# Kernel tuning notes

Measured on AMD Instinct MI355X. Metric: run time of the kernel, lower is better.

## Reference

```python
import jax, jax.numpy as jnp
import numpy as np

N_NODES = 50000
IN_DIM = 128
OUT_DIM = 128
HEADS = 4
HEAD_DIM = OUT_DIM // HEADS
N_EDGES = 800000
LN_EPS = 1e-5
NEG_SLOPE = 0.2


def setup_inputs() -> dict:
    key = jax.random.key(0)
    ks = jax.random.split(key, 8)
    x = jax.random.normal(ks[0], (N_NODES, IN_DIM), dtype=jnp.float32)
    edge_index = jax.random.randint(ks[1], (2, N_EDGES), 0, N_NODES, dtype=jnp.int64)
    s = 1.0 / np.sqrt(IN_DIM)
    W = jax.random.uniform(ks[2], (IN_DIM, HEADS * HEAD_DIM), jnp.float32, -s, s)
    att_src = jax.random.uniform(ks[3], (HEADS, HEAD_DIM), jnp.float32, -s, s)
    att_dst = jax.random.uniform(ks[4], (HEADS, HEAD_DIM), jnp.float32, -s, s)
    bias = jnp.zeros((OUT_DIM,), jnp.float32)
    gamma = jnp.ones((OUT_DIM,), jnp.float32)
    beta = jnp.zeros((OUT_DIM,), jnp.float32)
    return {"x": x, "edge_index": edge_index, "W": W, "att_src": att_src,
            "att_dst": att_dst, "bias": bias, "gamma": gamma, "beta": beta}


def reference(x, edge_index, W, att_src, att_dst, bias, gamma, beta):
    N = x.shape[0]
    H, C = att_src.shape
    # add self-loops (PyG GATConv default)
    loops = jnp.arange(N, dtype=edge_index.dtype)
    src = jnp.concatenate([edge_index[0], loops])  # [E+N]
    dst = jnp.concatenate([edge_index[1], loops])

    h = (x @ W).reshape(N, H, C)                      # [N,H,C]
    a_src = jnp.einsum('nhc,hc->nh', h, att_src)      # [N,H]
    a_dst = jnp.einsum('nhc,hc->nh', h, att_dst)

    e = jax.nn.leaky_relu(a_src[src] + a_dst[dst], NEG_SLOPE)   # [E+N,H]
    emax = jax.ops.segment_max(e, dst, num_segments=N)          # [N,H]
    ex = jnp.exp(e - emax[dst])
    denom = jax.ops.segment_sum(ex, dst, num_segments=N)
    alpha = ex / denom[dst]                                     # [E+N,H]

    msg = h[src] * alpha[:, :, None]                            # [E+N,H,C]
    out = jax.ops.segment_sum(msg, dst, num_segments=N).reshape(N, H * C) + bias

    # LayerNorm
    mu = out.mean(-1, keepdims=True)
    var = ((out - mu) ** 2).mean(-1, keepdims=True)
    hn = (out - mu) / jnp.sqrt(var + LN_EPS) * gamma + beta

    # residual is Identity (in_dim == out_dim); GELU exact; dropout = eval identity
    return jax.nn.gelu(hn + x, approximate=False)
```

## Files before the change

### kernel.cpp

```cpp
#include <hip/hip_runtime.h>
#include <math.h>

#define N_NODES 50000
#define HEADS 4
#define NEG_SLOPE 0.2f
#define LN_EPS 1e-5f
#define SLOTS 80
#define GR 64
#define EPB 2048
#define DSH 8
#define NB 196
#define CAP 40

typedef short short8 __attribute__((ext_vector_type(8)));
typedef float f32x4 __attribute__((ext_vector_type(4)));


__device__ __forceinline__ short f2bf(float f) {
    unsigned u = __float_as_uint(f);
    return (short)((u + 0x7fffu + ((u >> 16) & 1u)) >> 16);
}

__device__ __forceinline__ int detect_is64(const int* __restrict__ ei, int t, int* s_flag) {
    if (t < 64) {
        int nz = (ei[2 * t + 1] != 0) ? 1 : 0;
        unsigned long long b = __ballot(nz);
        if (t == 0) *s_flag = (b == 0ULL) ? 1 : 0;
    }
    __syncthreads();
    return *s_flag;
}

__device__ __forceinline__ float u8f(unsigned u, int p) {
    return (float)((u >> (8 * p)) & 0xffu);
}

__device__ __forceinline__ float edge_w(float v) {
    v = v > 0.f ? v : NEG_SLOPE * v;
    return __expf(v);
}


__global__ __launch_bounds__(256, 4) void gemm_scatter_kernel(
    const float* __restrict__ x, const float* __restrict__ W,
    const float* __restrict__ att_src, const float* __restrict__ att_dst,
    unsigned* __restrict__ hb, float* __restrict__ rec, float* __restrict__ a_dst,
    const int* __restrict__ ei, int E, int nScatter, int nGemm,
    unsigned* __restrict__ staging, int* __restrict__ scnt) {
    __shared__ __align__(16) char smem[40960];
    const int t = threadIdx.x;
    const int b = (int)blockIdx.x;

    const bool isBin = (b % 3) == 0;
    const int rid = isBin ? (b / 3) : (2 * (b / 3) + (b % 3) - 1);

    if (isBin) {
        if (rid >= nScatter) return;
        int is64 = detect_is64(ei, t, (int*)smem);
        int* lcnt = (int*)smem + 64;
        unsigned* cells = (unsigned*)(smem + 1056);
        for (int i = t; i < NB; i += 256) lcnt[i] = 0;
        __syncthreads();

        const int e0 = rid * EPB + t * 8;
        int ss[8], dd[8];
        if (e0 + 8 <= E) {
            if (is64) {
                const uint4* ps4 = (const uint4*)(ei + 2 * (size_t)e0);
                const uint4* pd4 = (const uint4*)(ei + 2 * ((size_t)E + e0));
#pragma unroll
                for (int u = 0; u < 4; ++u) {
                    uint4 qs = ps4[u], qd = pd4[u];
                    ss[2 * u] = (int)qs.x; ss[2 * u + 1] = (int)qs.z;
                    dd[2 * u] = (int)qd.x; dd[2 * u + 1] = (int)qd.z;
                }
            } else {
                const uint4* ps4 = (const uint4*)(ei + e0);
                const uint4* pd4 = (const uint4*)(ei + (size_t)E + e0);
#pragma unroll
                for (int u = 0; u < 2; ++u) {
                    uint4 qs = ps4[u], qd = pd4[u];
                    ss[4 * u] = (int)qs.x; ss[4 * u + 1] = (int)qs.y;
                    ss[4 * u + 2] = (int)qs.z; ss[4 * u + 3] = (int)qs.w;
                    dd[4 * u] = (int)qd.x; dd[4 * u + 1] = (int)qd.y;
                    dd[4 * u + 2] = (int)qd.z; dd[4 * u + 3] = (int)qd.w;
                }
            }
        } else {
#pragma unroll
            for (int u = 0; u < 8; ++u) {
                int e = e0 + u;
                if (e < E) {
                    if (is64) { ss[u] = ei[2 * e]; dd[u] = ei[2 * (E + e)]; }
                    else      { ss[u] = ei[e];     dd[u] = ei[E + e]; }
                } else { ss[u] = -1; dd[u] = 0; }
            }
        }
#pragma unroll
        for (int u = 0; u < 8; ++u) {
            if (ss[u] < 0) continue;
            int bkt = dd[u] >> DSH;
            int p = atomicAdd(&lcnt[bkt], 1);
            if (p < CAP)
                cells[bkt * CAP + p] = (unsigned)ss[u] | ((unsigned)dd[u] << 16);
        }
        __syncthreads();
        uint4* dst4 = (uint4*)(staging + (size_t)rid * NB * CAP);
        const uint4* src4 = (const uint4*)cells;
        for (int i = t; i < NB * CAP / 4; i += 256) dst4[i] = src4[i];
        for (int i = t; i < NB; i += 256)
            scnt[(size_t)rid * NB + i] = min(lcnt[i], CAP);
        return;
    }

    if (rid >= nGemm) return;
    const int rowBase = rid * GR;
    const int l = t & 63;
    const int wv = t >> 6;

    {
        const int nlo = l & 7, khi = l >> 3;
        for (int i = 0; i < 8; ++i) {
            int tile = wv + 4 * i;
            int n = (tile & 15) * 8 + nlo;
            int k8 = (tile >> 4) * 8 + khi;
            short8 pk;
#pragma unroll
            for (int jj = 0; jj < 8; ++jj)
                pk[jj] = f2bf(W[(k8 * 8 + jj) * 128 + n]);
            int us = (k8 & 8) | ((k8 & 7) ^ (n & 7));
            *(short8*)(smem + n * 256 + us * 16) = pk;
        }
    }
    __syncthreads();

    const int g = l >> 4;
    const int c = l & 15;

    f32x4 acc[8];
#pragma unroll
    for (int ct = 0; ct < 8; ++ct) acc[ct] = {0.f, 0.f, 0.f, 0.f};

    {
        int arow = rowBase + wv * 16 + c;
        if (arow >= N_NODES) arow = N_NODES - 1;
        const float* xrow = x + (size_t)arow * 128;
#pragma unroll
        for (int kk = 0; kk < 4; ++kk) {
            float4 xa = *(const float4*)(xrow + kk * 32 + g * 8);
            float4 xb = *(const float4*)(xrow + kk * 32 + g * 8 + 4);
            short8 af;
            af[0] = f2bf(xa.x); af[1] = f2bf(xa.y); af[2] = f2bf(xa.z); af[3] = f2bf(xa.w);
            af[4] = f2bf(xb.x); af[5] = f2bf(xb.y); af[6] = f2bf(xb.z); af[7] = f2bf(xb.w);
#pragma unroll
            for (int ct = 0; ct < 8; ++ct) {
                int n = ct * 16 + c;
                int u = kk * 4 + g;
                int us = (u & 8) | ((u & 7) ^ (n & 7));
                short8 bf = *(const short8*)(smem + n * 256 + us * 16);
                acc[ct] = __builtin_amdgcn_mfma_f32_16x16x32_bf16(af, bf, acc[ct], 0, 0, 0);
            }
        }
    }

    char* ep = smem + 32768 + wv * 2048;
    float asA[4], asB[4], adA[4], adB[4];
#pragma unroll
    for (int h = 0; h < 4; ++h) {
        asA[h] = att_src[h * 32 + c];
        asB[h] = att_src[h * 32 + 16 + c];
        adA[h] = att_dst[h * 32 + c];
        adB[h] = att_dst[h * 32 + 16 + c];
    }
#pragma unroll
    for (int r = 0; r < 4; ++r) {
        float v[8];
#pragma unroll
        for (int ct = 0; ct < 8; ++ct) v[ct] = acc[ct][r];

        float m = fabsf(v[0]);
#pragma unroll
        for (int ct = 1; ct < 8; ++ct) m = fmaxf(m, fabsf(v[ct]));
#pragma unroll
        for (int o = 1; o < 16; o <<= 1) m = fmaxf(m, __shfl_xor(m, o, 64));
        m = fmaxf(m, 1e-20f);
        const float inv = 127.0f / m;

        float sp[4], dp[4];
#pragma unroll
        for (int h = 0; h < 4; ++h) {
            sp[h] = v[2 * h] * asA[h] + v[2 * h + 1] * asB[h];
            dp[h] = v[2 * h] * adA[h] + v[2 * h + 1] * adB[h];
        }
#pragma unroll
        for (int o = 1; o < 16; o <<= 1) {
#pragma unroll
            for (int h = 0; h < 4; ++h) {
                sp[h] += __shfl_xor(sp[h], o, 64);
                dp[h] += __shfl_xor(dp[h], o, 64);
            }
        }
        const int row_l = g * 4 + r;
        const int row = rowBase + wv * 16 + row_l;
        if (c == 0 && row < N_NODES) {
            const float hs = m * (1.0f / 127.0f);
            float4* rw = (float4*)(rec + (size_t)row * 8);
            rw[0] = make_float4(sp[0], hs, sp[1], hs);
            rw[1] = make_float4(sp[2], hs, sp[3], hs);
            a_dst[row * 4 + 0] = dp[0]; a_dst[row * 4 + 1] = dp[1];
            a_dst[row * 4 + 2] = dp[2]; a_dst[row * 4 + 3] = dp[3];
        }
#pragma unroll
        for (int ct = 0; ct < 8; ++ct) {
            int q = __float2int_rn(v[ct] * inv);
            ep[row_l * 128 + ct * 16 + c] = (char)(q + 128);
        }
    }

#pragma unroll
    for (int w8 = 0; w8 < 8; ++w8) {
        int idx = w8 * 64 + l;
        int row_l = idx >> 5, tx = idx & 31;
        unsigned word = *(const unsigned*)(ep + row_l * 128 + tx * 4);
        int row = rowBase + wv * 16 + row_l;
        if (row < N_NODES) hb[(size_t)row * 32 + tx] = word;
    }
}

__global__ __launch_bounds__(256) void gat_fused_kernel(
    const unsigned* __restrict__ staging, const int* __restrict__ scnt, int nScatter,
    const float* __restrict__ rec, const float* __restrict__ a_dst,
    const unsigned* __restrict__ hb,
    const float* __restrict__ bias, const float* __restrict__ x,
    const float* __restrict__ gamma, const float* __restrict__ beta,
    float* __restrict__ out) {
    __shared__ __align__(16) unsigned short lists[16 * SLOTS];
    __shared__ int lcnt[16];
    const int t = threadIdx.x;
    const int n0 = blockIdx.x * 16;
    const int B = n0 >> DSH;
    const int grp16 = n0 >> 4;

    if (t < 16) lcnt[t] = 0;
    __syncthreads();

    for (int blk = t; blk < nScatter; blk += 256) {
        const int c = scnt[(size_t)blk * NB + B];
        const unsigned* cell = staging + ((size_t)blk * NB + B) * CAP;
        for (int j = 0; j < c; j += 4) {
            uint4 q = *(const uint4*)(cell + j);
            const int m = c - j;
            {
                int d = (int)(q.x >> 16);
                if ((d >> 4) == grp16) {
                    int p = atomicAdd(&lcnt[d & 15], 1);
                    if (p < SLOTS) lists[(d & 15) * SLOTS + p] = (unsigned short)(q.x & 0xffffu);
                }
            }
            if (m > 1) {
                int d = (int)(q.y >> 16);
                if ((d >> 4) == grp16) {
                    int p = atomicAdd(&lcnt[d & 15], 1);
                    if (p < SLOTS) lists[(d & 15) * SLOTS + p] = (unsigned short)(q.y & 0xffffu);
                }
            }
            if (m > 2) {
                int d = (int)(q.z >> 16);
                if ((d >> 4) == grp16) {
                    int p = atomicAdd(&lcnt[d & 15], 1);
                    if (p < SLOTS) lists[(d & 15) * SLOTS + p] = (unsigned short)(q.z & 0xffffu);
                }
            }
            if (m > 3) {
                int d = (int)(q.w >> 16);
                if ((d >> 4) == grp16) {
                    int p = atomicAdd(&lcnt[d & 15], 1);
                    if (p < SLOTS) lists[(d & 15) * SLOTS + p] = (unsigned short)(q.w & 0xffffu);
                }
            }
        }
    }
    __syncthreads();

    const int l = t & 63;
    const int wv = t >> 6;
    const int g = l >> 4;
    const int j = l & 15;
    const int li = wv * 4 + g;
    const int n = n0 + li;
    const int hh = j >> 2;

    const uint2* hb2 = (const uint2*)hb;
    const uint2* rec2 = (const uint2*)rec;

    const float adst_me = a_dst[(n << 2) + hh];
    uint2 rS = rec2[(unsigned)(n * 4 + hh)];
    float ps = edge_w(__uint_as_float(rS.x) + adst_me);

    uint2 hvS = hb2[(unsigned)(n * 16 + j)];
    {
        const float uS = ps * __uint_as_float(rS.y);
        float su = uS;
        float acc0 = uS * u8f(hvS.x, 0), acc1 = uS * u8f(hvS.x, 1);
        float acc2 = uS * u8f(hvS.x, 2), acc3 = uS * u8f(hvS.x, 3);
        float acc4 = uS * u8f(hvS.y, 0), acc5 = uS * u8f(hvS.y, 1);
        float acc6 = uS * u8f(hvS.y, 2), acc7 = uS * u8f(hvS.y, 3);

        const int deg = min(lcnt[li], SLOTS);
        const unsigned short* row = lists + li * SLOTS;

        for (int base = 0; base < deg; base += 8) {
            const int rem = deg - base;
            uint4 q = *(const uint4*)(row + base);
            int s0 = (int)(q.x & 0xffffu);
            int s1 = (rem > 1) ? (int)(q.x >> 16) : n;
            int s2 = (rem > 2) ? (int)(q.y & 0xffffu) : n;
            int s3 = (rem > 3) ? (int)(q.y >> 16) : n;
            int s4 = (rem > 4) ? (int)(q.z & 0xffffu) : n;
            int s5 = (rem > 5) ? (int)(q.z >> 16) : n;
            int s6 = (rem > 6) ? (int)(q.w & 0xffffu) : n;
            int s7 = (rem > 7) ? (int)(q.w >> 16) : n;

            uint2 r0 = rec2[(unsigned)(s0 * 4 + hh)];
            uint2 r1 = rec2[(unsigned)(s1 * 4 + hh)];
            uint2 r2 = rec2[(unsigned)(s2 * 4 + hh)];
            uint2 r3 = rec2[(unsigned)(s3 * 4 + hh)];
            uint2 r4 = rec2[(unsigned)(s4 * 4 + hh)];
            uint2 r5 = rec2[(unsigned)(s5 * 4 + hh)];
            uint2 r6 = rec2[(unsigned)(s6 * 4 + hh)];
            uint2 r7 = rec2[(unsigned)(s7 * 4 + hh)];
            uint2 h0 = hb2[(unsigned)(s0 * 16 + j)];
            uint2 h1 = hb2[(unsigned)(s1 * 16 + j)];
            uint2 h2 = hb2[(unsigned)(s2 * 16 + j)];
            uint2 h3 = hb2[(unsigned)(s3 * 16 + j)];
            uint2 h4 = hb2[(unsigned)(s4 * 16 + j)];
            uint2 h5 = hb2[(unsigned)(s5 * 16 + j)];
            uint2 h6 = hb2[(unsigned)(s6 * 16 + j)];
            uint2 h7 = hb2[(unsigned)(s7 * 16 + j)];

            float w0 = edge_w(__uint_as_float(r0.x) + adst_me);
            float w1 = (rem > 1) ? edge_w(__uint_as_float(r1.x) + adst_me) : 0.f;
            float w2 = (rem > 2) ? edge_w(__uint_as_float(r2.x) + adst_me) : 0.f;
            float w3 = (rem > 3) ? edge_w(__uint_as_float(r3.x) + adst_me) : 0.f;
            float w4 = (rem > 4) ? edge_w(__uint_as_float(r4.x) + adst_me) : 0.f;
            float w5 = (rem > 5) ? edge_w(__uint_as_float(r5.x) + adst_me) : 0.f;
            float w6 = (rem > 6) ? edge_w(__uint_as_float(r6.x) + adst_me) : 0.f;
            float w7 = (rem > 7) ? edge_w(__uint_as_float(r7.x) + adst_me) : 0.f;
            ps += (w0 + w1 + w2 + w3) + (w4 + w5 + w6 + w7);

            float u0 = w0 * __uint_as_float(r0.y), u1 = w1 * __uint_as_float(r1.y);
            float u2 = w2 * __uint_as_float(r2.y), u3 = w3 * __uint_as_float(r3.y);
            float u4 = w4 * __uint_as_float(r4.y), u5 = w5 * __uint_as_float(r5.y);
            float u6 = w6 * __uint_as_float(r6.y), u7 = w7 * __uint_as_float(r7.y);
            su += (u0 + u1 + u2 + u3) + (u4 + u5 + u6 + u7);

            acc0 += u0 * u8f(h0.x, 0) + u1 * u8f(h1.x, 0) + u2 * u8f(h2.x, 0) + u3 * u8f(h3.x, 0)
                  + u4 * u8f(h4.x, 0) + u5 * u8f(h5.x, 0) + u6 * u8f(h6.x, 0) + u7 * u8f(h7.x, 0);
            acc1 += u0 * u8f(h0.x, 1) + u1 * u8f(h1.x, 1) + u2 * u8f(h2.x, 1) + u3 * u8f(h3.x, 1)
                  + u4 * u8f(h4.x, 1) + u5 * u8f(h5.x, 1) + u6 * u8f(h6.x, 1) + u7 * u8f(h7.x, 1);
            acc2 += u0 * u8f(h0.x, 2) + u1 * u8f(h1.x, 2) + u2 * u8f(h2.x, 2) + u3 * u8f(h3.x, 2)
                  + u4 * u8f(h4.x, 2) + u5 * u8f(h5.x, 2) + u6 * u8f(h6.x, 2) + u7 * u8f(h7.x, 2);
            acc3 += u0 * u8f(h0.x, 3) + u1 * u8f(h1.x, 3) + u2 * u8f(h2.x, 3) + u3 * u8f(h3.x, 3)
                  + u4 * u8f(h4.x, 3) + u5 * u8f(h5.x, 3) + u6 * u8f(h6.x, 3) + u7 * u8f(h7.x, 3);
            acc4 += u0 * u8f(h0.y, 0) + u1 * u8f(h1.y, 0) + u2 * u8f(h2.y, 0) + u3 * u8f(h3.y, 0)
                  + u4 * u8f(h4.y, 0) + u5 * u8f(h5.y, 0) + u6 * u8f(h6.y, 0) + u7 * u8f(h7.y, 0);
            acc5 += u0 * u8f(h0.y, 1) + u1 * u8f(h1.y, 1) + u2 * u8f(h2.y, 1) + u3 * u8f(h3.y, 1)
                  + u4 * u8f(h4.y, 1) + u5 * u8f(h5.y, 1) + u6 * u8f(h6.y, 1) + u7 * u8f(h7.y, 1);
            acc6 += u0 * u8f(h0.y, 2) + u1 * u8f(h1.y, 2) + u2 * u8f(h2.y, 2) + u3 * u8f(h3.y, 2)
                  + u4 * u8f(h4.y, 2) + u5 * u8f(h5.y, 2) + u6 * u8f(h6.y, 2) + u7 * u8f(h7.y, 2);
            acc7 += u0 * u8f(h0.y, 3) + u1 * u8f(h1.y, 3) + u2 * u8f(h2.y, 3) + u3 * u8f(h3.y, 3)
                  + u4 * u8f(h4.y, 3) + u5 * u8f(h5.y, 3) + u6 * u8f(h6.y, 3) + u7 * u8f(h7.y, 3);
        }

        const float inv = 1.0f / ps;
        const float cs = 128.0f * su;
        const float4* bias4 = (const float4*)bias;
        float4 bA = bias4[j * 2], bB = bias4[j * 2 + 1];
        float v0 = (acc0 - cs) * inv + bA.x, v1 = (acc1 - cs) * inv + bA.y;
        float v2 = (acc2 - cs) * inv + bA.z, v3 = (acc3 - cs) * inv + bA.w;
        float v4 = (acc4 - cs) * inv + bB.x, v5 = (acc5 - cs) * inv + bB.y;
        float v6 = (acc6 - cs) * inv + bB.z, v7 = (acc7 - cs) * inv + bB.w;

        float s1 = v0 + v1 + v2 + v3 + v4 + v5 + v6 + v7;
        float s2 = v0 * v0 + v1 * v1 + v2 * v2 + v3 * v3 +
                   v4 * v4 + v5 * v5 + v6 * v6 + v7 * v7;
#pragma unroll
        for (int o = 1; o < 16; o <<= 1) {
            s1 += __shfl_xor(s1, o, 64);
            s2 += __shfl_xor(s2, o, 64);
        }
        float mu = s1 * (1.0f / 128.0f);
        float var = s2 * (1.0f / 128.0f) - mu * mu;
        float rstd = rsqrtf(var + LN_EPS);

        const float4* gamma4 = (const float4*)gamma;
        const float4* beta4 = (const float4*)beta;
        const float4* x4 = (const float4*)x;
        float4 gA = gamma4[j * 2], gB = gamma4[j * 2 + 1];
        float4 eA = beta4[j * 2], eB = beta4[j * 2 + 1];
        float4 xA = x4[(size_t)n * 32 + j * 2], xB = x4[(size_t)n * 32 + j * 2 + 1];

        float r0f = (v0 - mu) * rstd * gA.x + eA.x + xA.x;
        float r1f = (v1 - mu) * rstd * gA.y + eA.y + xA.y;
        float r2f = (v2 - mu) * rstd * gA.z + eA.z + xA.z;
        float r3f = (v3 - mu) * rstd * gA.w + eA.w + xA.w;
        float r4f = (v4 - mu) * rstd * gB.x + eB.x + xB.x;
        float r5f = (v5 - mu) * rstd * gB.y + eB.y + xB.y;
        float r6f = (v6 - mu) * rstd * gB.z + eB.z + xB.z;
        float r7f = (v7 - mu) * rstd * gB.w + eB.w + xB.w;

        const float k = 0.70710678118654752440f;
        float4 oA = make_float4(0.5f * r0f * (1.0f + erff(r0f * k)),
                                0.5f * r1f * (1.0f + erff(r1f * k)),
                                0.5f * r2f * (1.0f + erff(r2f * k)),
                                0.5f * r3f * (1.0f + erff(r3f * k)));
        float4 oB = make_float4(0.5f * r4f * (1.0f + erff(r4f * k)),
                                0.5f * r5f * (1.0f + erff(r5f * k)),
                                0.5f * r6f * (1.0f + erff(r6f * k)),
                                0.5f * r7f * (1.0f + erff(r7f * k)));
        float4* out4 = (float4*)out;
        out4[(size_t)n * 32 + j * 2] = oA;
        out4[(size_t)n * 32 + j * 2 + 1] = oB;
    }
}


extern "C" void kernel_launch(void* const* d_in, const int* in_sizes, int n_in,
                              void* d_out, int out_size, void* d_ws, size_t ws_size,
                              hipStream_t stream) {
    const float* x       = (const float*)d_in[0];
    const int*   ei      = (const int*)d_in[1];
    const float* W       = (const float*)d_in[2];
    const float* att_src = (const float*)d_in[3];
    const float* att_dst = (const float*)d_in[4];
    const float* bias    = (const float*)d_in[5];
    const float* gamma   = (const float*)d_in[6];
    const float* beta    = (const float*)d_in[7];
    float* out = (float*)d_out;
    const int E = in_sizes[1] / 2;

    unsigned* hb         = (unsigned*)d_ws;
    float* rec           = (float*)(hb + (size_t)N_NODES * 32);
    float* a_dst         = rec + (size_t)N_NODES * 8;

    const int nScatter = (E + EPB - 1) / EPB;
    unsigned* staging    = (unsigned*)(a_dst + (size_t)N_NODES * 4);
    int* scnt            = (int*)(staging + (size_t)nScatter * NB * CAP);

    const int nGemm = (N_NODES + GR - 1) / GR;
    int total = 3 * nScatter;
    const int needGemm = 3 * ((nGemm + 1) / 2);
    if (needGemm > total) total = needGemm;

    gemm_scatter_kernel<<<total, 256, 0, stream>>>(
        x, W, att_src, att_dst, hb, rec, a_dst, ei, E, nScatter, nGemm,
        staging, scnt);
    gat_fused_kernel<<<N_NODES / 16, 256, 0, stream>>>(staging, scnt, nScatter,
                                                       rec, a_dst, hb,
                                                       bias, x, gamma, beta, out);
}
```

Measured before the change: 160.9 us.

## Split adjacency list build into separate kernel and prefetch x before W staging

Before this change, every 16-node block of the fused aggregation kernel rescanned the full staging bucket for its 256-node range, filtering for its own nodes. A new build_kernel scans each bucket once and writes per-node counts and source lists to global memory, and the aggregation kernel then reads them directly. This removes the roughly 16-fold redundant staging scan, at the cost of an extra launch and a global write and read of the edge lists. Separately, the GEMM path loads the x rows into registers before staging W into shared memory, so the load latencies overlap.

```diff
diff --git a/kernel.cpp b/kernel.cpp
--- a/kernel.cpp
+++ b/kernel.cpp
@@ -118,6 +118,21 @@
     const int l = t & 63;
     const int wv = t >> 6;
 
+    const int g = l >> 4;
+    const int c = l & 15;
+
+    float4 xr[8];
+    {
+        int arow = rowBase + wv * 16 + c;
+        if (arow >= N_NODES) arow = N_NODES - 1;
+        const float* xrow = x + (size_t)arow * 128;
+#pragma unroll
+        for (int kk = 0; kk < 4; ++kk) {
+            xr[2 * kk]     = *(const float4*)(xrow + kk * 32 + g * 8);
+            xr[2 * kk + 1] = *(const float4*)(xrow + kk * 32 + g * 8 + 4);
+        }
+    }
+
     {
         const int nlo = l & 7, khi = l >> 3;
         for (int i = 0; i < 8; ++i) {
@@ -134,32 +149,23 @@
     }
     __syncthreads();
 
-    const int g = l >> 4;
-    const int c = l & 15;
-
     f32x4 acc[8];
 #pragma unroll
     for (int ct = 0; ct < 8; ++ct) acc[ct] = {0.f, 0.f, 0.f, 0.f};
 
-    {
-        int arow = rowBase + wv * 16 + c;
-        if (arow >= N_NODES) arow = N_NODES - 1;
-        const float* xrow = x + (size_t)arow * 128;
-#pragma unroll
-        for (int kk = 0; kk < 4; ++kk) {
-            float4 xa = *(const float4*)(xrow + kk * 32 + g * 8);
-            float4 xb = *(const float4*)(xrow + kk * 32 + g * 8 + 4);
-            short8 af;
-            af[0] = f2bf(xa.x); af[1] = f2bf(xa.y); af[2] = f2bf(xa.z); af[3] = f2bf(xa.w);
-            af[4] = f2bf(xb.x); af[5] = f2bf(xb.y); af[6] = f2bf(xb.z); af[7] = f2bf(xb.w);
-#pragma unroll
-            for (int ct = 0; ct < 8; ++ct) {
-                int n = ct * 16 + c;
-                int u = kk * 4 + g;
-                int us = (u & 8) | ((u & 7) ^ (n & 7));
-                short8 bf = *(const short8*)(smem + n * 256 + us * 16);
-                acc[ct] = __builtin_amdgcn_mfma_f32_16x16x32_bf16(af, bf, acc[ct], 0, 0, 0);
-            }
+#pragma unroll
+    for (int kk = 0; kk < 4; ++kk) {
+        float4 xa = xr[2 * kk], xb = xr[2 * kk + 1];
+        short8 af;
+        af[0] = f2bf(xa.x); af[1] = f2bf(xa.y); af[2] = f2bf(xa.z); af[3] = f2bf(xa.w);
+        af[4] = f2bf(xb.x); af[5] = f2bf(xb.y); af[6] = f2bf(xb.z); af[7] = f2bf(xb.w);
+#pragma unroll
+        for (int ct = 0; ct < 8; ++ct) {
+            int n = ct * 16 + c;
+            int u = kk * 4 + g;
+            int us = (u & 8) | ((u & 7) ^ (n & 7));
+            short8 bf = *(const short8*)(smem + n * 256 + us * 16);
+            acc[ct] = __builtin_amdgcn_mfma_f32_16x16x32_bf16(af, bf, acc[ct], 0, 0, 0);
         }
     }
 
@@ -227,21 +233,13 @@
     }
 }
 
-__global__ __launch_bounds__(256) void gat_fused_kernel(
-    const unsigned* __restrict__ staging, const int* __restrict__ scnt, int nScatter,
-    const float* __restrict__ rec, const float* __restrict__ a_dst,
-    const unsigned* __restrict__ hb,
-    const float* __restrict__ bias, const float* __restrict__ x,
-    const float* __restrict__ gamma, const float* __restrict__ beta,
-    float* __restrict__ out) {
-    __shared__ __align__(16) unsigned short lists[16 * SLOTS];
-    __shared__ int lcnt[16];
+__global__ __launch_bounds__(256) void build_kernel(
+    const unsigned* __restrict__ staging, const int* __restrict__ scnt,
+    int nScatter, int* __restrict__ cnt, unsigned short* __restrict__ esrc) {
+    __shared__ int lcnt2[256];
+    const int B = blockIdx.x;
     const int t = threadIdx.x;
-    const int n0 = blockIdx.x * 16;
-    const int B = n0 >> DSH;
-    const int grp16 = n0 >> 4;
-
-    if (t < 16) lcnt[t] = 0;
+    lcnt2[t] = 0;
     __syncthreads();
 
     for (int blk = t; blk < nScatter; blk += 256) {
@@ -252,42 +250,44 @@
             const int m = c - j;
             {
                 int d = (int)(q.x >> 16);
-                if ((d >> 4) == grp16) {
-                    int p = atomicAdd(&lcnt[d & 15], 1);
-                    if (p < SLOTS) lists[(d & 15) * SLOTS + p] = (unsigned short)(q.x & 0xffffu);
-                }
+                int p = atomicAdd(&lcnt2[d & 255], 1);
+                if (p < SLOTS) esrc[(size_t)d * SLOTS + p] = (unsigned short)(q.x & 0xffffu);
             }
             if (m > 1) {
                 int d = (int)(q.y >> 16);
-                if ((d >> 4) == grp16) {
-                    int p = atomicAdd(&lcnt[d & 15], 1);
-                    if (p < SLOTS) lists[(d & 15) * SLOTS + p] = (unsigned short)(q.y & 0xffffu);
-                }
+                int p = atomicAdd(&lcnt2[d & 255], 1);
+                if (p < SLOTS) esrc[(size_t)d * SLOTS + p] = (unsigned short)(q.y & 0xffffu);
             }
             if (m > 2) {
                 int d = (int)(q.z >> 16);
-                if ((d >> 4) == grp16) {
-                    int p = atomicAdd(&lcnt[d & 15], 1);
-                    if (p < SLOTS) lists[(d & 15) * SLOTS + p] = (unsigned short)(q.z & 0xffffu);
-                }
+                int p = atomicAdd(&lcnt2[d & 255], 1);
+                if (p < SLOTS) esrc[(size_t)d * SLOTS + p] = (unsigned short)(q.z & 0xffffu);
             }
             if (m > 3) {
                 int d = (int)(q.w >> 16);
-                if ((d >> 4) == grp16) {
-                    int p = atomicAdd(&lcnt[d & 15], 1);
-                    if (p < SLOTS) lists[(d & 15) * SLOTS + p] = (unsigned short)(q.w & 0xffffu);
-                }
+                int p = atomicAdd(&lcnt2[d & 255], 1);
+                if (p < SLOTS) esrc[(size_t)d * SLOTS + p] = (unsigned short)(q.w & 0xffffu);
             }
         }
     }
     __syncthreads();
-
+    const int d = (B << DSH) + t;
+    if (d < N_NODES) cnt[d] = lcnt2[t];
+}
+
+__global__ __launch_bounds__(256) void gat_fused_kernel(
+    const int* __restrict__ cnt, const unsigned short* __restrict__ esrc,
+    const float* __restrict__ rec, const float* __restrict__ a_dst,
+    const unsigned* __restrict__ hb,
+    const float* __restrict__ bias, const float* __restrict__ x,
+    const float* __restrict__ gamma, const float* __restrict__ beta,
+    float* __restrict__ out) {
+    const int t = threadIdx.x;
     const int l = t & 63;
     const int wv = t >> 6;
     const int g = l >> 4;
     const int j = l & 15;
-    const int li = wv * 4 + g;
-    const int n = n0 + li;
+    const int n = blockIdx.x * 16 + wv * 4 + g;
     const int hh = j >> 2;
 
     const uint2* hb2 = (const uint2*)hb;
@@ -306,8 +306,8 @@
         float acc4 = uS * u8f(hvS.y, 0), acc5 = uS * u8f(hvS.y, 1);
         float acc6 = uS * u8f(hvS.y, 2), acc7 = uS * u8f(hvS.y, 3);
 
-        const int deg = min(lcnt[li], SLOTS);
-        const unsigned short* row = lists + li * SLOTS;
+        const int deg = min(cnt[n], SLOTS);
+        const unsigned short* row = esrc + n * SLOTS;
 
         for (int base = 0; base < deg; base += 8) {
             const int rem = deg - base;
@@ -442,9 +442,11 @@
     unsigned* hb         = (unsigned*)d_ws;
     float* rec           = (float*)(hb + (size_t)N_NODES * 32);
     float* a_dst         = rec + (size_t)N_NODES * 8;
+    int*   cnt           = (int*)(a_dst + N_NODES * 4);
+    unsigned short* esrc = (unsigned short*)(cnt + N_NODES);
 
     const int nScatter = (E + EPB - 1) / EPB;
-    unsigned* staging    = (unsigned*)(a_dst + (size_t)N_NODES * 4);
+    unsigned* staging    = (unsigned*)(esrc + (size_t)N_NODES * SLOTS);
     int* scnt            = (int*)(staging + (size_t)nScatter * NB * CAP);
 
     const int nGemm = (N_NODES + GR - 1) / GR;
@@ -455,7 +457,7 @@
     gemm_scatter_kernel<<<total, 256, 0, stream>>>(
         x, W, att_src, att_dst, hb, rec, a_dst, ei, E, nScatter, nGemm,
         staging, scnt);
-    gat_fused_kernel<<<N_NODES / 16, 256, 0, stream>>>(staging, scnt, nScatter,
-                                                       rec, a_dst, hb,
+    build_kernel<<<NB, 256, 0, stream>>>(staging, scnt, nScatter, cnt, esrc);
+    gat_fused_kernel<<<N_NODES / 16, 256, 0, stream>>>(cnt, esrc, rec, a_dst, hb,
                                                        bias, x, gamma, beta, out);
 }
```

Result: faster. 149.1 us (-7.3%).
